# Performance work log

Measured on AMD Instinct MI355X. Metric: run time of the kernel, lower is better.

Reference implementation:

```python
import jax, jax.numpy as jnp
import numpy as np

D_MODEL = 2048
N_HEADS = 16
HEAD_DIM = 128
WINDOW = 512
ROPE_BASE = 10000.0
B, N = 2, 2048
INNER = N_HEADS * HEAD_DIM


def setup_inputs() -> dict:
    key = jax.random.key(0)
    k1, k2, k3 = jax.random.split(key, 3)
    x = jax.random.normal(k1, (B, N, D_MODEL), dtype=jnp.float32)
    # torch nn.Linear stores weight as [out_features, in_features]
    w_qkv = jax.random.normal(k2, (3 * INNER, D_MODEL), dtype=jnp.float32) / np.sqrt(D_MODEL)
    w_o = jax.random.normal(k3, (D_MODEL, INNER), dtype=jnp.float32) / np.sqrt(INNER)
    return {"x": x, "w_qkv": w_qkv, "w_o": w_o}


def _rotate_half(t):
    t1, t2 = jnp.split(t, 2, axis=-1)
    return jnp.concatenate([-t2, t1], axis=-1)


def _rope(q, k, offset=0):
    # q, k: [B, H, N, D]; GPT-NeoX half-split rotary embedding
    D = q.shape[-1]
    inv_freq = 1.0 / (ROPE_BASE ** (jnp.arange(0, D, 2, dtype=jnp.float32) / D))
    pos = jnp.arange(q.shape[2], dtype=jnp.float32) + offset
    ang = pos[:, None] * inv_freq[None, :]                 # [N, D/2]
    cos = jnp.concatenate([jnp.cos(ang), jnp.cos(ang)], axis=-1)  # [N, D]
    sin = jnp.concatenate([jnp.sin(ang), jnp.sin(ang)], axis=-1)
    q_r = q * cos + _rotate_half(q) * sin
    k_r = k * cos + _rotate_half(k) * sin
    return q_r, k_r


def reference(x, w_qkv, w_o):
    Bq, Nq, _ = x.shape
    # QKV projection (no bias)
    qkv = jnp.einsum('bnd,ed->bne', x, w_qkv)              # [B, N, 3*INNER]
    q, k, v = jnp.split(qkv, 3, axis=-1)
    def to_heads(t):
        return t.reshape(Bq, Nq, N_HEADS, HEAD_DIM).transpose(0, 2, 1, 3)  # [B,H,N,D]
    q, k, v = to_heads(q), to_heads(k), to_heads(v)
    q, k = _rope(q, k, offset=0)
    # sliding-window causal mask: valid key j for query i iff (i - WINDOW) < j <= i
    i = jnp.arange(Nq)[:, None]
    j = jnp.arange(Nq)[None, :]
    valid = (j > i - WINDOW) & (j <= i)                    # [N, N]
    scale = 1.0 / np.sqrt(HEAD_DIM)
    scores = jnp.einsum('bhnd,bhkd->bhnk', q, k) * scale   # [B,H,N,N]
    scores = jnp.where(valid[None, None], scores, -jnp.inf)
    att = jax.nn.softmax(scores, axis=-1)
    out = jnp.einsum('bhnk,bhkd->bhnd', att, v)
    out = out.transpose(0, 2, 1, 3).reshape(Bq, Nq, INNER)
    y = jnp.einsum('bni,di->bnd', out, w_o)
    return y
```

## Files before the change

kernel.cpp:

```cpp
#include <hip/hip_runtime.h>
#include <hip/hip_bf16.h>
#include <cstdint>

typedef __bf16 bf16x8 __attribute__((ext_vector_type(8)));
typedef float floatx4 __attribute__((ext_vector_type(4)));

__device__ __forceinline__ void gl2lds16(const void* g, void* l) {
  __builtin_amdgcn_global_load_lds(
      (const __attribute__((address_space(1))) unsigned int*)g,
      (__attribute__((address_space(3))) unsigned int*)(uintptr_t)l,
      16, 0, 0);
}

__global__ __launch_bounds__(256)
void cvt_kernel(const float* __restrict__ in, __hip_bfloat16* __restrict__ out, int n) {
  int i = (blockIdx.x * 256 + threadIdx.x) * 4;
  if (i >= n) return;
  const float4 v = *(const float4*)(in + i);
  out[i + 0] = __float2bfloat16(v.x);
  out[i + 1] = __float2bfloat16(v.y);
  out[i + 2] = __float2bfloat16(v.z);
  out[i + 3] = __float2bfloat16(v.w);
}

__global__ __launch_bounds__(256)
void gemm_bt(const __hip_bfloat16* __restrict__ A, const __hip_bfloat16* __restrict__ Bm,
             void* __restrict__ Cp, int M, int Nc, int K, int c_fp32)
{
  __shared__ __hip_bfloat16 As[128 * 32];
  __shared__ __hip_bfloat16 Bs[128 * 32];
  const int tid = threadIdx.x;
  const int lane = tid & 63, wave = tid >> 6;
  const int wm = (wave & 1) * 64, wn = (wave >> 1) * 64;
  const int m0 = blockIdx.x * 128, n0 = blockIdx.y * 128;
  const int lrow = lane & 15, lk = (lane >> 4) * 8;
  floatx4 acc[4][4] = {};
  const int c0 = tid, c1 = tid + 256;
  const int r0 = c0 >> 2, o0 = (c0 & 3) * 8;
  const int r1 = c1 >> 2, o1 = (c1 & 3) * 8;
  for (int kt = 0; kt < K; kt += 32) {
    __syncthreads();
    gl2lds16(A + (size_t)(m0 + r0) * K + kt + o0, &As[c0 * 8]);
    gl2lds16(A + (size_t)(m0 + r1) * K + kt + o1, &As[c1 * 8]);
    gl2lds16(Bm + (size_t)(n0 + r0) * K + kt + o0, &Bs[c0 * 8]);
    gl2lds16(Bm + (size_t)(n0 + r1) * K + kt + o1, &Bs[c1 * 8]);
    __syncthreads();
    bf16x8 af[4], bfr[4];
#pragma unroll
    for (int t = 0; t < 4; t++) af[t] = *(const bf16x8*)&As[(wm + t * 16 + lrow) * 32 + lk];
#pragma unroll
    for (int t = 0; t < 4; t++) bfr[t] = *(const bf16x8*)&Bs[(wn + t * 16 + lrow) * 32 + lk];
#pragma unroll
    for (int mt = 0; mt < 4; mt++)
#pragma unroll
      for (int nt = 0; nt < 4; nt++)
        acc[mt][nt] = __builtin_amdgcn_mfma_f32_16x16x32_bf16(af[mt], bfr[nt], acc[mt][nt], 0, 0, 0);
  }
  const int lq4 = (lane >> 4) * 4;
#pragma unroll
  for (int mt = 0; mt < 4; mt++)
#pragma unroll
    for (int nt = 0; nt < 4; nt++)
#pragma unroll
      for (int r = 0; r < 4; r++) {
        const int m = m0 + wm + mt * 16 + lq4 + r;
        const int n = n0 + wn + nt * 16 + lrow;
        const float v = acc[mt][nt][r];
        if (c_fp32) ((float*)Cp)[(size_t)m * Nc + n] = v;
        else ((__hip_bfloat16*)Cp)[(size_t)m * Nc + n] = __float2bfloat16(v);
      }
}

__global__ __launch_bounds__(256)
void gemm_qkv_fused(const __hip_bfloat16* __restrict__ A,
                    const __hip_bfloat16* __restrict__ W,
                    __hip_bfloat16* __restrict__ Qr,
                    __hip_bfloat16* __restrict__ Kr,
                    __hip_bfloat16* __restrict__ Vt)
{
  __shared__ alignas(16) char smem[16640];
  __shared__ float invf[64];
  __hip_bfloat16* As = (__hip_bfloat16*)smem;
  __hip_bfloat16* Bs = As + 128 * 32;
  __hip_bfloat16* Cs = (__hip_bfloat16*)smem;
  const int tid = threadIdx.x;
  if (tid < 64) invf[tid] = __expf(-(float)tid * 0.14391156831212787f);
  const int lane = tid & 63, wave = tid >> 6;
  const int wm = (wave & 1) * 64, wn = (wave >> 1) * 64;
  const int m0 = blockIdx.x * 128, n0 = blockIdx.y * 128;
  const int K = 2048;
  const int lrow = lane & 15, lk = (lane >> 4) * 8;
  floatx4 acc[4][4] = {};
  const int c0 = tid, c1 = tid + 256;
  const int r0 = c0 >> 2, o0 = (c0 & 3) * 8;
  const int r1 = c1 >> 2, o1 = (c1 & 3) * 8;
  for (int kt = 0; kt < K; kt += 32) {
    __syncthreads();
    gl2lds16(A + (size_t)(m0 + r0) * K + kt + o0, &As[c0 * 8]);
    gl2lds16(A + (size_t)(m0 + r1) * K + kt + o1, &As[c1 * 8]);
    gl2lds16(W + (size_t)(n0 + r0) * K + kt + o0, &Bs[c0 * 8]);
    gl2lds16(W + (size_t)(n0 + r1) * K + kt + o1, &Bs[c1 * 8]);
    __syncthreads();
    bf16x8 af[4], bfr[4];
#pragma unroll
    for (int t = 0; t < 4; t++) af[t] = *(const bf16x8*)&As[(wm + t * 16 + lrow) * 32 + lk];
#pragma unroll
    for (int t = 0; t < 4; t++) bfr[t] = *(const bf16x8*)&Bs[(wn + t * 16 + lrow) * 32 + lk];
#pragma unroll
    for (int mt = 0; mt < 4; mt++)
#pragma unroll
      for (int nt = 0; nt < 4; nt++)
        acc[mt][nt] = __builtin_amdgcn_mfma_f32_16x16x32_bf16(af[mt], bfr[nt], acc[mt][nt], 0, 0, 0);
  }
  const int lq4 = (lane >> 4) * 4;
  const int seg = n0 >> 11;
  const int h = (n0 & 2047) >> 7;
  const int b = m0 >> 11;
  const int bh = b * 16 + h;
  const int seq0 = m0 & 2047;
  const float qscale = (seg == 0) ? 0.08838834764831845f : 1.0f;
  for (int pass = 0; pass < 2; ++pass) {
    __syncthreads();
    if ((wave & 1) == pass) {
#pragma unroll
      for (int mt = 0; mt < 4; mt++)
#pragma unroll
        for (int nt = 0; nt < 4; nt++)
#pragma unroll
          for (int r = 0; r < 4; r++)
            Cs[(mt * 16 + lq4 + r) * 130 + wn + nt * 16 + lrow] =
                __float2bfloat16(acc[mt][nt][r]);
    }
    __syncthreads();
    if (seg < 2) {
      __hip_bfloat16* Out = seg ? Kr : Qr;
#pragma unroll
      for (int p = 0; p < 2; ++p) {
        const int row = (tid >> 3) + p * 32;
        const int oct = (tid & 7) * 8;
        const int m = m0 + pass * 64 + row;
        const float pos = (float)(m & 2047);
        alignas(16) __hip_bfloat16 lo[8], hi[8];
#pragma unroll
        for (int k2 = 0; k2 < 8; k2++) {
          const float ang = pos * invf[oct + k2];
          float sn, cs2;
          __sincosf(ang, &sn, &cs2);
          const float a  = __bfloat162float(Cs[row * 130 + oct + k2]);
          const float bb = __bfloat162float(Cs[row * 130 + oct + k2 + 64]);
          lo[k2] = __float2bfloat16((a * cs2 - bb * sn) * qscale);
          hi[k2] = __float2bfloat16((bb * cs2 + a * sn) * qscale);
        }
        const size_t ob = ((size_t)bh * 2048 + (size_t)(m & 2047)) * 128;
        *(bf16x8*)&Out[ob + oct]      = *(const bf16x8*)lo;
        *(bf16x8*)&Out[ob + oct + 64] = *(const bf16x8*)hi;
      }
    } else {
#pragma unroll
      for (int p = 0; p < 4; ++p) {
        const int d = (tid >> 3) + p * 32;
        const int s8 = (tid & 7) * 8;
        alignas(16) __hip_bfloat16 tmp[8];
#pragma unroll
        for (int k2 = 0; k2 < 8; k2++) tmp[k2] = Cs[(s8 + k2) * 130 + d];
        const size_t ob = ((size_t)bh * 128 + d) * 2048 + seq0 + pass * 64 + s8;
        *(bf16x8*)&Vt[ob] = *(const bf16x8*)tmp;
      }
    }
  }
}

__global__ __launch_bounds__(512)
void attn_swa(const __hip_bfloat16* __restrict__ Qr, const __hip_bfloat16* __restrict__ Kr,
              const __hip_bfloat16* __restrict__ Vt, __hip_bfloat16* __restrict__ Out)
{
  __shared__ __hip_bfloat16 Ks[64 * 128];
  __shared__ __hip_bfloat16 Vs[128 * 64];
  __shared__ __hip_bfloat16 Pb[8][16 * 72];
  const int qt = blockIdx.x, bh = blockIdx.y;
  const int tid = threadIdx.x, lane = tid & 63, wave = tid >> 6;
  const int lrow = lane & 15, lk = (lane >> 4) * 8, lq4 = (lane >> 4) * 4;
  const int i0 = qt * 128;
  const float NEG_INF = -__builtin_inff();
  const __hip_bfloat16* Qh = Qr + (size_t)bh * 2048 * 128;
  const __hip_bfloat16* Kh = Kr + (size_t)bh * 2048 * 128;
  const __hip_bfloat16* Vh = Vt + (size_t)bh * 128 * 2048;

#pragma unroll
  for (int it = 0; it < 4; it++) {
    const int c = it * 512 + tid;
    __hip_bfloat16* dst = (c < 1024) ? &Ks[c * 8] : &Vs[(c - 1024) * 8];
    gl2lds16(Qh + (size_t)(i0 + (c >> 4)) * 128 + (c & 15) * 8, dst);
  }
  __syncthreads();
  bf16x8 qf[4];
  {
    const __hip_bfloat16* qbuf = (wave < 4) ? Ks : Vs;
    const int qrow = (wave & 3) * 16 + lrow;
#pragma unroll
    for (int ks = 0; ks < 4; ks++)
      qf[ks] = *(const bf16x8*)&qbuf[qrow * 128 + ks * 32 + lk];
  }

  floatx4 accO[8] = {};
  float m_i = NEG_INF, l_i = 0.f;
  const int iw = i0 + wave * 16 + lrow;
  const int imin = i0 + wave * 16;
  const int lo = i0 - 511;
  const int jt_lo = (lo > 0 ? lo : 0) >> 6;
  const int jt_hi = (i0 + 127) >> 6;

  for (int jt = jt_lo; jt <= jt_hi; jt++) {
    const int j0 = jt * 64;
    __syncthreads();
#pragma unroll
    for (int it = 0; it < 2; it++) {
      const int c = it * 512 + tid;
      gl2lds16(Kh + (size_t)(j0 + (c >> 4)) * 128 + (c & 15) * 8, &Ks[c * 8]);
      gl2lds16(Vh + (size_t)(c >> 3) * 2048 + j0 + (c & 7) * 8, &Vs[c * 8]);
    }
    __syncthreads();
    floatx4 s[4] = {};
#pragma unroll
    for (int nt = 0; nt < 4; nt++)
#pragma unroll
      for (int ks = 0; ks < 4; ks++) {
        const bf16x8 kf = *(const bf16x8*)&Ks[(nt * 16 + lrow) * 128 + ks * 32 + lk];
        s[nt] = __builtin_amdgcn_mfma_f32_16x16x32_bf16(kf, qf[ks], s[nt], 0, 0, 0);
      }
    const bool full = (j0 + 63 <= imin) && (j0 >= imin + 15 - 511);
    float rmax = NEG_INF;
    if (full) {
#pragma unroll
      for (int nt = 0; nt < 4; nt++)
#pragma unroll
        for (int r = 0; r < 4; r++) rmax = fmaxf(rmax, s[nt][r]);
    } else {
#pragma unroll
      for (int nt = 0; nt < 4; nt++) {
#pragma unroll
        for (int r = 0; r < 4; r++) {
          const int j = j0 + nt * 16 + lq4 + r;
          const float sv = ((j <= iw) && (j > iw - 512)) ? s[nt][r] : NEG_INF;
          s[nt][r] = sv;
          rmax = fmaxf(rmax, sv);
        }
      }
    }
    rmax = fmaxf(rmax, __shfl_xor(rmax, 16));
    rmax = fmaxf(rmax, __shfl_xor(rmax, 32));
    const float mnew = fmaxf(m_i, rmax);
    const float alpha = __expf(fminf(m_i - mnew, 0.f));
    m_i = mnew;
    float rs = 0.f;
    if (full) {
#pragma unroll
      for (int nt = 0; nt < 4; nt++)
#pragma unroll
        for (int r = 0; r < 4; r++) {
          const float p = __expf(s[nt][r] - mnew);
          s[nt][r] = p;
          rs += p;
        }
    } else {
#pragma unroll
      for (int nt = 0; nt < 4; nt++)
#pragma unroll
        for (int r = 0; r < 4; r++) {
          const float sv = s[nt][r];
          const float p = (sv == NEG_INF) ? 0.f : __expf(sv - mnew);
          s[nt][r] = p;
          rs += p;
        }
    }
    rs += __shfl_xor(rs, 16);
    rs += __shfl_xor(rs, 32);
    l_i = l_i * alpha + rs;
#pragma unroll
    for (int dt = 0; dt < 8; dt++) accO[dt] *= alpha;
#pragma unroll
    for (int nt = 0; nt < 4; nt++) {
      alignas(8) __hip_bfloat16 p4[4];
#pragma unroll
      for (int r = 0; r < 4; r++) p4[r] = __float2bfloat16(s[nt][r]);
      *(uint64_t*)&Pb[wave][lrow * 72 + nt * 16 + lq4] = *(const uint64_t*)p4;
    }
    bf16x8 pf[2];
#pragma unroll
    for (int jf = 0; jf < 2; jf++)
      pf[jf] = *(const bf16x8*)&Pb[wave][lrow * 72 + jf * 32 + lk];
#pragma unroll
    for (int dt = 0; dt < 8; dt++)
#pragma unroll
      for (int jf = 0; jf < 2; jf++) {
        const bf16x8 vf = *(const bf16x8*)&Vs[(dt * 16 + lrow) * 64 + jf * 32 + lk];
        accO[dt] = __builtin_amdgcn_mfma_f32_16x16x32_bf16(vf, pf[jf], accO[dt], 0, 0, 0);
      }
  }
  const int b = bh >> 4, h = bh & 15;
  const float inv_l = 1.0f / l_i;
  const size_t rowb = ((size_t)(b * 2048 + iw)) * 2048 + h * 128;
#pragma unroll
  for (int dt = 0; dt < 8; dt++) {
    alignas(8) __hip_bfloat16 o4[4];
#pragma unroll
    for (int r = 0; r < 4; r++) o4[r] = __float2bfloat16(accO[dt][r] * inv_l);
    *(uint64_t*)&Out[rowb + dt * 16 + lq4] = *(const uint64_t*)o4;
  }
}

extern "C" void kernel_launch(void* const* d_in, const int* in_sizes, int n_in,
                              void* d_out, int out_size, void* d_ws, size_t ws_size,
                              hipStream_t stream)
{
  const float* x = (const float*)d_in[0];
  const float* w_qkv = (const float*)d_in[1];
  const float* w_o = (const float*)d_in[2];
  float* y = (float*)d_out;
  char* ws = (char*)d_ws;

  const size_t SZ_X = 16777216;
  const size_t SZ_WQKV = 25165824;
  const size_t SZ_Q = 16777216;

  __hip_bfloat16* xb = (__hip_bfloat16*)(ws);
  __hip_bfloat16* wqkvb = (__hip_bfloat16*)(ws + SZ_X);
  __hip_bfloat16* Qr = (__hip_bfloat16*)(ws + SZ_X + SZ_WQKV);
  __hip_bfloat16* Kr = (__hip_bfloat16*)(ws + SZ_X + SZ_WQKV + SZ_Q);
  __hip_bfloat16* Vt = (__hip_bfloat16*)(ws + SZ_X + SZ_WQKV + 2 * SZ_Q);

  cvt_kernel<<<dim3(8192), dim3(256), 0, stream>>>(x, xb, 8388608);
  cvt_kernel<<<dim3(12288), dim3(256), 0, stream>>>(w_qkv, wqkvb, 12582912);
  gemm_qkv_fused<<<dim3(32, 48), dim3(256), 0, stream>>>(xb, wqkvb, Qr, Kr, Vt);
  attn_swa<<<dim3(16, 32), dim3(512), 0, stream>>>(Qr, Kr, Vt, xb );
  cvt_kernel<<<dim3(4096), dim3(256), 0, stream>>>(w_o, wqkvb, 4194304);
  gemm_bt<<<dim3(32, 16), dim3(256), 0, stream>>>(xb, wqkvb, (void*)y, 4096, 2048, 2048, 1);
}
```

Baseline: 399.3 us.

## Load K/V fragments directly from global memory in sliding-window attention

The attention kernel no longer stages K and V tiles through shared memory with block-wide barriers. Each wave now reads its MFMA operands straight from global memory, which relies on L1/L2 caching for reuse across waves. The query tile shrinks from 128 to 64 rows with 256-thread blocks, doubling the grid and dropping LDS use to allow more resident blocks. This removes the barrier and LDS staging cost, but repeated K/V reads per wave now go through the cache hierarchy with less coalescing and more global traffic.

```diff
diff --git a/kernel.cpp b/kernel.cpp
--- a/kernel.cpp
+++ b/kernel.cpp
@@ -170,64 +170,45 @@
   }
 }
 
-__global__ __launch_bounds__(512)
+__global__ __launch_bounds__(256, 4)
 void attn_swa(const __hip_bfloat16* __restrict__ Qr, const __hip_bfloat16* __restrict__ Kr,
               const __hip_bfloat16* __restrict__ Vt, __hip_bfloat16* __restrict__ Out)
 {
-  __shared__ __hip_bfloat16 Ks[64 * 128];
-  __shared__ __hip_bfloat16 Vs[128 * 64];
-  __shared__ __hip_bfloat16 Pb[8][16 * 72];
+  __shared__ __hip_bfloat16 Pb[4][16 * 72];
   const int qt = blockIdx.x, bh = blockIdx.y;
   const int tid = threadIdx.x, lane = tid & 63, wave = tid >> 6;
   const int lrow = lane & 15, lk = (lane >> 4) * 8, lq4 = (lane >> 4) * 4;
-  const int i0 = qt * 128;
+  const int i0 = qt * 64;
   const float NEG_INF = -__builtin_inff();
   const __hip_bfloat16* Qh = Qr + (size_t)bh * 2048 * 128;
   const __hip_bfloat16* Kh = Kr + (size_t)bh * 2048 * 128;
   const __hip_bfloat16* Vh = Vt + (size_t)bh * 128 * 2048;
 
-#pragma unroll
-  for (int it = 0; it < 4; it++) {
-    const int c = it * 512 + tid;
-    __hip_bfloat16* dst = (c < 1024) ? &Ks[c * 8] : &Vs[(c - 1024) * 8];
-    gl2lds16(Qh + (size_t)(i0 + (c >> 4)) * 128 + (c & 15) * 8, dst);
-  }
-  __syncthreads();
+  const int iw = i0 + wave * 16 + lrow;
   bf16x8 qf[4];
-  {
-    const __hip_bfloat16* qbuf = (wave < 4) ? Ks : Vs;
-    const int qrow = (wave & 3) * 16 + lrow;
-#pragma unroll
-    for (int ks = 0; ks < 4; ks++)
-      qf[ks] = *(const bf16x8*)&qbuf[qrow * 128 + ks * 32 + lk];
-  }
+#pragma unroll
+  for (int ks = 0; ks < 4; ks++)
+    qf[ks] = *(const bf16x8*)&Qh[(size_t)iw * 128 + ks * 32 + lk];
 
   floatx4 accO[8] = {};
   float m_i = NEG_INF, l_i = 0.f;
-  const int iw = i0 + wave * 16 + lrow;
   const int imin = i0 + wave * 16;
   const int lo = i0 - 511;
   const int jt_lo = (lo > 0 ? lo : 0) >> 6;
-  const int jt_hi = (i0 + 127) >> 6;
+  const int jt_hi = i0 >> 6;
 
   for (int jt = jt_lo; jt <= jt_hi; jt++) {
     const int j0 = jt * 64;
-    __syncthreads();
-#pragma unroll
-    for (int it = 0; it < 2; it++) {
-      const int c = it * 512 + tid;
-      gl2lds16(Kh + (size_t)(j0 + (c >> 4)) * 128 + (c & 15) * 8, &Ks[c * 8]);
-      gl2lds16(Vh + (size_t)(c >> 3) * 2048 + j0 + (c & 7) * 8, &Vs[c * 8]);
-    }
-    __syncthreads();
     floatx4 s[4] = {};
 #pragma unroll
-    for (int nt = 0; nt < 4; nt++)
+    for (int nt = 0; nt < 4; nt++) {
+      const size_t krow = (size_t)(j0 + nt * 16 + lrow) * 128;
 #pragma unroll
       for (int ks = 0; ks < 4; ks++) {
-        const bf16x8 kf = *(const bf16x8*)&Ks[(nt * 16 + lrow) * 128 + ks * 32 + lk];
+        const bf16x8 kf = *(const bf16x8*)&Kh[krow + ks * 32 + lk];
         s[nt] = __builtin_amdgcn_mfma_f32_16x16x32_bf16(kf, qf[ks], s[nt], 0, 0, 0);
       }
+    }
     const bool full = (j0 + 63 <= imin) && (j0 >= imin + 15 - 511);
     float rmax = NEG_INF;
     if (full) {
@@ -290,12 +271,14 @@
     for (int jf = 0; jf < 2; jf++)
       pf[jf] = *(const bf16x8*)&Pb[wave][lrow * 72 + jf * 32 + lk];
 #pragma unroll
-    for (int dt = 0; dt < 8; dt++)
+    for (int dt = 0; dt < 8; dt++) {
+      const size_t vrow = (size_t)(dt * 16 + lrow) * 2048 + j0;
 #pragma unroll
       for (int jf = 0; jf < 2; jf++) {
-        const bf16x8 vf = *(const bf16x8*)&Vs[(dt * 16 + lrow) * 64 + jf * 32 + lk];
+        const bf16x8 vf = *(const bf16x8*)&Vh[vrow + jf * 32 + lk];
         accO[dt] = __builtin_amdgcn_mfma_f32_16x16x32_bf16(vf, pf[jf], accO[dt], 0, 0, 0);
       }
+    }
   }
   const int b = bh >> 4, h = bh & 15;
   const float inv_l = 1.0f / l_i;
@@ -332,7 +315,7 @@
   cvt_kernel<<<dim3(8192), dim3(256), 0, stream>>>(x, xb, 8388608);
   cvt_kernel<<<dim3(12288), dim3(256), 0, stream>>>(w_qkv, wqkvb, 12582912);
   gemm_qkv_fused<<<dim3(32, 48), dim3(256), 0, stream>>>(xb, wqkvb, Qr, Kr, Vt);
-  attn_swa<<<dim3(16, 32), dim3(512), 0, stream>>>(Qr, Kr, Vt, xb );
+  attn_swa<<<dim3(32, 32), dim3(256), 0, stream>>>(Qr, Kr, Vt, xb );
   cvt_kernel<<<dim3(4096), dim3(256), 0, stream>>>(w_o, wqkvb, 4194304);
   gemm_bt<<<dim3(32, 16), dim3(256), 0, stream>>>(xb, wqkvb, (void*)y, 4096, 2048, 2048, 1);
 }
```

Result: slower. 459.7 us (+15.1%).
